# Kernel optimization log

Measured on AMD Instinct MI355X. Metric: run time of the kernel, lower is better.

The kernel has to match this reference:

```python
import jax, jax.numpy as jnp
import numpy as np


def _shift2d(x, dh, dw):
    """Return y with y[..., h, w] = x[..., h+dh, w+dw], zero-padded out of bounds."""
    B, C, H, W = x.shape
    ph, pw = abs(dh), abs(dw)
    xp = jnp.pad(x, ((0, 0), (0, 0), (ph, ph), (pw, pw)))
    return xp[:, :, ph + dh: ph + dh + H, pw + dw: pw + dw + W]


def setup_inputs() -> dict:
    key = jax.random.key(0)
    k1, k2 = jax.random.split(key)
    B, C_in, C_out, K, H, W = 64, 16, 16, 3, 256, 256
    x = jax.random.normal(k1, (B, C_in, H, W), dtype=jnp.float32)
    fan_in = C_in * K
    bound = np.sqrt(2.0) * np.sqrt(3.0 / fan_in)  # kaiming_uniform, relu
    weight = jax.random.uniform(k2, (C_out, C_in, K), dtype=jnp.float32,
                                minval=-bound, maxval=bound)
    return {"x": x, "weight": weight, "dilation": 1, "step": 0}


def reference(x, weight, dilation, step):
    # Skeleton conv: 1D kernel of size K swept over a 2D map, stride 1,
    # same-padded (output spatial size == input spatial size).
    # Tap k samples input at (h + (k-K//2)*step, w + (k-K//2)*dilation).
    K = weight.shape[2]
    c0 = K // 2
    B, C, H, W = x.shape
    out = jnp.zeros((B, weight.shape[0], H, W), dtype=x.dtype)
    for k in range(K):  # K is a small static constant
        off = k - c0
        xs = _shift2d(x, off * step, off * dilation)  # [B,C,H,W] gathered taps
        out = out + jnp.einsum("oc,bchw->bohw", weight[:, :, k], xs)
    return out
```

## Files before the change

kernel.cpp:

```cpp
#include <hip/hip_runtime.h>


constexpr int CIN = 16, COUT = 16, KK = 3, H = 256, W = 256;
constexpr int WT  = 4;
constexpr int TPR = W / WT;

typedef float f4 __attribute__((ext_vector_type(4)));

__global__ __launch_bounds__(256)
void skel_conv_kernel(const float* __restrict__ x, const float* __restrict__ wgt,
                      const int* __restrict__ dil_p, const int* __restrict__ step_p,
                      float* __restrict__ out, int B)
{
    const int dil  = dil_p[0];
    const int step = step_p[0];

    const int tid  = blockIdx.x * blockDim.x + threadIdx.x;
    const int lane = tid & (TPR - 1);
    const int h    = (tid / TPR) & (H - 1);
    const int b    = tid / (TPR * H);
    if (b >= B) return;
    const int w0 = lane * WT;

    float acc[COUT][WT];
    #pragma unroll
    for (int o = 0; o < COUT; ++o)
        #pragma unroll
        for (int j = 0; j < WT; ++j) acc[o][j] = 0.f;

    const size_t xbase = (size_t)b * CIN * H * W;

    if (dil == 1 && step == 0) {
        for (int c = 0; c < CIN; ++c) {
            const float* xr = x + xbase + (size_t)c * (H * W) + (size_t)h * W;
            f4 v = *(const f4*)(xr + w0);
            float left  = __shfl_up(v.w, 1);
            float right = __shfl_down(v.x, 1);
            if (lane == 0)       left  = 0.f;
            if (lane == TPR - 1) right = 0.f;

            const float t0[WT] = {left, v.x, v.y, v.z};
            const float t1[WT] = {v.x,  v.y, v.z, v.w};
            const float t2[WT] = {v.y,  v.z, v.w, right};

            #pragma unroll
            for (int o = 0; o < COUT; ++o) {
                const float wk0 = wgt[(o * CIN + c) * KK + 0];
                const float wk1 = wgt[(o * CIN + c) * KK + 1];
                const float wk2 = wgt[(o * CIN + c) * KK + 2];
                #pragma unroll
                for (int j = 0; j < WT; ++j)
                    acc[o][j] += wk0 * t0[j] + wk1 * t1[j] + wk2 * t2[j];
            }
        }
    } else {
        for (int c = 0; c < CIN; ++c) {
            const float* xc = x + xbase + (size_t)c * (H * W);
            #pragma unroll
            for (int k = 0; k < KK; ++k) {
                const int off = k - KK / 2;
                const int hh  = h + off * step;
                const bool rowok = (hh >= 0) && (hh < H);
                const int hcl = hh < 0 ? 0 : (hh > H - 1 ? H - 1 : hh);
                float t[WT];
                #pragma unroll
                for (int j = 0; j < WT; ++j) {
                    const int ww  = w0 + j + off * dil;
                    const bool ok = rowok && (ww >= 0) && (ww < W);
                    const int wcl = ww < 0 ? 0 : (ww > W - 1 ? W - 1 : ww);
                    const float v = xc[(size_t)hcl * W + wcl];
                    t[j] = ok ? v : 0.f;
                }
                #pragma unroll
                for (int o = 0; o < COUT; ++o) {
                    const float wk = wgt[(o * CIN + c) * KK + k];
                    #pragma unroll
                    for (int j = 0; j < WT; ++j)
                        acc[o][j] += wk * t[j];
                }
            }
        }
    }

    float* orow = out + ((size_t)b * COUT * H + h) * W + w0;
    #pragma unroll
    for (int o = 0; o < COUT; ++o) {
        f4 r = {acc[o][0], acc[o][1], acc[o][2], acc[o][3]};
        *(f4*)(orow + (size_t)o * (H * W)) = r;
    }
}

extern "C" void kernel_launch(void* const* d_in, const int* in_sizes, int n_in,
                              void* d_out, int out_size, void* d_ws, size_t ws_size,
                              hipStream_t stream) {
    const float* x    = (const float*)d_in[0];
    const float* wgt  = (const float*)d_in[1];
    const int*   dil  = (const int*)d_in[2];
    const int*   step = (const int*)d_in[3];
    float*       out  = (float*)d_out;

    const int B = in_sizes[0] / (CIN * H * W);
    const int total = B * H * TPR;
    const int block = 256;
    const int grid  = (total + block - 1) / block;

    skel_conv_kernel<<<grid, block, 0, stream>>>(x, wgt, dil, step, out, B);
}
```

Before: 141.7 us.

## Stage input rows in LDS via async global_load_lds, one pixel per thread

Each block now handles one (b,h) row. It loads all 16 input-channel rows into shared memory with the direct global-to-LDS load builtin, then each thread computes one output pixel by reading its left, centre and right neighbours from LDS. This replaces the earlier layout of 4 pixels per thread with wave shuffles. Because each thread produces one pixel instead of four, weights are reloaded per pixel, stores become scalar, and far more blocks are launched. The gain depends on whether the kernel is memory-bound, which it is (about 33MB in and 33MB out).

New measurement: 365.5 us. 2.58x slower.

```diff
diff --git a/kernel.cpp b/kernel.cpp
--- a/kernel.cpp
+++ b/kernel.cpp
@@ -2,10 +2,12 @@
 
 
 constexpr int CIN = 16, COUT = 16, KK = 3, H = 256, W = 256;
-constexpr int WT  = 4;
-constexpr int TPR = W / WT;
 
-typedef float f4 __attribute__((ext_vector_type(4)));
+__device__ __forceinline__ void load_lds16(const float* g, float* l) {
+    __builtin_amdgcn_global_load_lds(
+        (const __attribute__((address_space(1))) void*)g,
+        (__attribute__((address_space(3))) void*)l, 16, 0, 0);
+}
 
 __global__ __launch_bounds__(256)
 void skel_conv_kernel(const float* __restrict__ x, const float* __restrict__ wgt,
@@ -15,79 +17,71 @@
     const int dil  = dil_p[0];
     const int step = step_p[0];
 
-    const int tid  = blockIdx.x * blockDim.x + threadIdx.x;
-    const int lane = tid & (TPR - 1);
-    const int h    = (tid / TPR) & (H - 1);
-    const int b    = tid / (TPR * H);
+    const int t   = threadIdx.x;
+    const int row = blockIdx.x;
+    const int h   = row & (H - 1);
+    const int b   = row >> 8;
     if (b >= B) return;
-    const int w0 = lane * WT;
+    const size_t cs = (size_t)H * W;
 
-    float acc[COUT][WT];
+    __shared__ float xs[CIN * W];
+
+    float acc[COUT];
     #pragma unroll
-    for (int o = 0; o < COUT; ++o)
-        #pragma unroll
-        for (int j = 0; j < WT; ++j) acc[o][j] = 0.f;
-
-    const size_t xbase = (size_t)b * CIN * H * W;
+    for (int o = 0; o < COUT; ++o) acc[o] = 0.f;
 
     if (dil == 1 && step == 0) {
+        const int ln = t & 63, wv = t >> 6;
+        const float* src = x + (size_t)b * CIN * cs + (size_t)h * W + ln * 4;
+        #pragma unroll
+        for (int i = 0; i < CIN / 4; ++i) {
+            const int c = wv * (CIN / 4) + i;
+            load_lds16(src + (size_t)c * cs, &xs[c * W]);
+        }
+        __syncthreads();
+
+        const int w  = t;
+        const int wm = (w == 0)     ? 0     : w - 1;
+        const int wp = (w == W - 1) ? W - 1 : w + 1;
+        #pragma unroll
         for (int c = 0; c < CIN; ++c) {
-            const float* xr = x + xbase + (size_t)c * (H * W) + (size_t)h * W;
-            f4 v = *(const f4*)(xr + w0);
-            float left  = __shfl_up(v.w, 1);
-            float right = __shfl_down(v.x, 1);
-            if (lane == 0)       left  = 0.f;
-            if (lane == TPR - 1) right = 0.f;
-
-            const float t0[WT] = {left, v.x, v.y, v.z};
-            const float t1[WT] = {v.x,  v.y, v.z, v.w};
-            const float t2[WT] = {v.y,  v.z, v.w, right};
-
+            const float* r = &xs[c * W];
+            float left  = r[wm];
+            float mid   = r[w];
+            float right = r[wp];
+            if (w == 0)     left  = 0.f;
+            if (w == W - 1) right = 0.f;
             #pragma unroll
             for (int o = 0; o < COUT; ++o) {
-                const float wk0 = wgt[(o * CIN + c) * KK + 0];
-                const float wk1 = wgt[(o * CIN + c) * KK + 1];
-                const float wk2 = wgt[(o * CIN + c) * KK + 2];
-                #pragma unroll
-                for (int j = 0; j < WT; ++j)
-                    acc[o][j] += wk0 * t0[j] + wk1 * t1[j] + wk2 * t2[j];
+                const float* wq = wgt + ((size_t)o * CIN + c) * KK;
+                acc[o] += wq[0] * left + wq[1] * mid + wq[2] * right;
             }
         }
     } else {
+        #pragma unroll 1
         for (int c = 0; c < CIN; ++c) {
-            const float* xc = x + xbase + (size_t)c * (H * W);
+            const float* xc = x + (size_t)b * CIN * cs + (size_t)c * cs;
             #pragma unroll
             for (int k = 0; k < KK; ++k) {
                 const int off = k - KK / 2;
                 const int hh  = h + off * step;
-                const bool rowok = (hh >= 0) && (hh < H);
+                const int ww  = t + off * dil;
+                const bool ok = (hh >= 0) && (hh < H) && (ww >= 0) && (ww < W);
                 const int hcl = hh < 0 ? 0 : (hh > H - 1 ? H - 1 : hh);
-                float t[WT];
+                const int wcl = ww < 0 ? 0 : (ww > W - 1 ? W - 1 : ww);
+                float v = xc[(size_t)hcl * W + wcl];
+                v = ok ? v : 0.f;
                 #pragma unroll
-                for (int j = 0; j < WT; ++j) {
-                    const int ww  = w0 + j + off * dil;
-                    const bool ok = rowok && (ww >= 0) && (ww < W);
-                    const int wcl = ww < 0 ? 0 : (ww > W - 1 ? W - 1 : ww);
-                    const float v = xc[(size_t)hcl * W + wcl];
-                    t[j] = ok ? v : 0.f;
-                }
-                #pragma unroll
-                for (int o = 0; o < COUT; ++o) {
-                    const float wk = wgt[(o * CIN + c) * KK + k];
-                    #pragma unroll
-                    for (int j = 0; j < WT; ++j)
-                        acc[o][j] += wk * t[j];
-                }
+                for (int o = 0; o < COUT; ++o)
+                    acc[o] += wgt[((size_t)o * CIN + c) * KK + k] * v;
             }
         }
     }
 
-    float* orow = out + ((size_t)b * COUT * H + h) * W + w0;
+    float* op = out + (size_t)b * COUT * cs + (size_t)h * W + t;
     #pragma unroll
-    for (int o = 0; o < COUT; ++o) {
-        f4 r = {acc[o][0], acc[o][1], acc[o][2], acc[o][3]};
-        *(f4*)(orow + (size_t)o * (H * W)) = r;
-    }
+    for (int o = 0; o < COUT; ++o)
+        op[(size_t)o * cs] = acc[o];
 }
 
 extern "C" void kernel_launch(void* const* d_in, const int* in_sizes, int n_in,
@@ -100,9 +94,6 @@
     float*       out  = (float*)d_out;
 
     const int B = in_sizes[0] / (CIN * H * W);
-    const int total = B * H * TPR;
-    const int block = 256;
-    const int grid  = (total + block - 1) / block;
-
-    skel_conv_kernel<<<grid, block, 0, stream>>>(x, wgt, dil, step, out, B);
+    const int grid = B * H;
+    skel_conv_kernel<<<grid, 256, 0, stream>>>(x, wgt, dil, step, out, B);
 }
```
